# Optimization experiments

Hardware: AMD Instinct MI355X
Metric: run time of the kernel (lower is better)

The kernel has to match this reference:

```python
import jax, jax.numpy as jnp
import numpy as np

B, D_MODEL, N, H = 4, 256, 2048, 4
HEAD_DIM = D_MODEL // H  # 64


def _rotate_half(x):
    # x: [..., d] with d even; pairs (x1, x2) -> (-x2, x1)
    x = x.reshape(x.shape[:-1] + (x.shape[-1] // 2, 2))
    x1, x2 = x[..., 0], x[..., 1]
    return jnp.stack((-x2, x1), axis=-1).reshape(x.shape[:-2] + (-1,))


def _apply_rope(freqs, t):
    # freqs: [2, n, d] (cos, sin); t: [b, h, n, d]
    return t * freqs[0] + _rotate_half(t) * freqs[1]


def setup_inputs() -> dict:
    key = jax.random.key(0)
    ks = jax.random.split(key, 12)
    s = 0.02
    inp = {
        "query": jax.random.normal(ks[0], (B, D_MODEL, N), jnp.float32),
        "key": jax.random.normal(ks[1], (B, D_MODEL, N), jnp.float32),
        "value": jax.random.normal(ks[2], (B, D_MODEL, N), jnp.float32),
        "encoding": jax.random.normal(ks[3], (2, N, HEAD_DIM), jnp.float32),
        "Wq": jax.random.normal(ks[4], (D_MODEL, D_MODEL), jnp.float32) * s,
        "bq": jnp.zeros((D_MODEL,), jnp.float32),
        "Wk": jax.random.normal(ks[5], (D_MODEL, D_MODEL), jnp.float32) * s,
        "bk": jnp.zeros((D_MODEL,), jnp.float32),
        "Wv": jax.random.normal(ks[6], (D_MODEL, D_MODEL), jnp.float32) * s,
        "bv": jnp.zeros((D_MODEL,), jnp.float32),
        "Wm": jax.random.normal(ks[7], (D_MODEL, D_MODEL), jnp.float32) * s,
        "bm": jnp.zeros((D_MODEL,), jnp.float32),
    }
    return inp


def _proj(W, b, x):
    # 1x1 Conv1d == channel matmul: x [b, c_in, n] -> [b, c_out, n]
    return jnp.einsum('oi,bin->bon', W, x) + b[None, :, None]


def reference(query, key, value, encoding, Wq, bq, Wk, bk, Wv, bv, Wm, bm):
    b = query.shape[0]
    # project and split channels into (head_dim, heads): [b, d, h, n]
    q = _proj(Wq, bq, query).reshape(b, HEAD_DIM, H, -1)
    k = _proj(Wk, bk, key).reshape(b, HEAD_DIM, H, -1)
    v = _proj(Wv, bv, value).reshape(b, HEAD_DIM, H, -1)
    # RoPE on [b, h, n, d] layout
    q = jnp.transpose(_apply_rope(encoding, jnp.transpose(q, (0, 2, 3, 1))), (0, 3, 1, 2))
    k = jnp.transpose(_apply_rope(encoding, jnp.transpose(k, (0, 2, 3, 1))), (0, 3, 1, 2))
    # attention: scores [b, h, n, m]
    scores = jnp.einsum('bdhn,bdhm->bhnm', q, k) / jnp.sqrt(jnp.float32(HEAD_DIM))
    prob = jax.nn.softmax(scores, axis=-1)
    x = jnp.einsum('bhnm,bdhm->bdhn', prob, v)
    x = x.reshape(b, HEAD_DIM * H, -1)
    return _proj(Wm, bm, x)
```

## Files before the change

kernel.cpp:

```cpp
#include <hip/hip_runtime.h>
#include <stdint.h>

#define NSEQ 2048

typedef __attribute__((ext_vector_type(4))) float f32x4;
typedef __attribute__((ext_vector_type(8))) short s16x8;
typedef _Float16 f16x8 __attribute__((ext_vector_type(8)));

#define OFF_XT  0u
#define OFF_XA  0u
#define OFF_PO  4194304u
#define OFF_W   12582912u
#define OFF_QR  13107200u
#define OFF_KR  17301504u
#define OFF_VT  21495808u
#define OFF_M   25690112u
#define OFF_L   25952256u

__device__ __forceinline__ short f2h(float f) {
  _Float16 h = (_Float16)f;
  return __builtin_bit_cast(short, h);
}
__device__ __forceinline__ float h2f(short s) {
  return (float)__builtin_bit_cast(_Float16, s);
}
__device__ __forceinline__ int swz64(int row, int slot) {
  return row * 64 + ((slot ^ ((row >> 1) & 3)) << 4);
}
__device__ __forceinline__ int swz128(int row, int slot) {
  return row * 128 + ((slot ^ (row & 7)) << 4);
}
#define MFMA(a, b, c) __builtin_amdgcn_mfma_f32_16x16x32_f16(a, b, c, 0, 0, 0)

__global__ void k_convw(const float* __restrict__ Wq, const float* __restrict__ Wk,
                        const float* __restrict__ Wv, const float* __restrict__ Wm,
                        char* __restrict__ ws) {
  int o = blockIdx.x, which = blockIdx.y, i = threadIdx.x;
  const float* src = which == 0 ? Wq : which == 1 ? Wk : which == 2 ? Wv : Wm;
  short* dst = (short*)(ws + OFF_W) + which * 65536;
  float val = (which < 3) ? src[o * 256 + i] : src[o * 256 + ((i & 63) << 2) + (i >> 6)];
  dst[o * 256 + i] = f2h(val);
}

__global__ __launch_bounds__(256) void k_trans(const float* __restrict__ q,
    const float* __restrict__ k, const float* __restrict__ v, char* __restrict__ ws) {
  int tensor = blockIdx.z >> 2, b = blockIdx.z & 3;
  const float* src = tensor == 0 ? q : (tensor == 1 ? k : v);
  short* dst = (short*)(ws + OFF_XT) + (tensor * 4 + b) * 524288;
  int n0 = blockIdx.x * 64, i0 = blockIdx.y * 64;
  __shared__ float tile[64][65];
  int t = threadIdx.x;
  int nl = t & 63, ib = (t >> 6) * 16;
#pragma unroll
  for (int r = 0; r < 16; ++r)
    tile[ib + r][nl] = src[(b * 256 + i0 + ib + r) * 2048 + n0 + nl];
  __syncthreads();
  int nr = t >> 2, ic = (t & 3) * 16;
  short tmp[16];
#pragma unroll
  for (int j = 0; j < 16; ++j) tmp[j] = f2h(tile[ic + j][nr]);
  short* dp = &dst[(n0 + nr) * 256 + i0 + ic];
  *(s16x8*)dp = *(const s16x8*)&tmp[0];
  *(s16x8*)(dp + 8) = *(const s16x8*)&tmp[8];
}

__device__ __forceinline__ void gemm128(const short* __restrict__ W, const short* __restrict__ X,
                                        int o0, int n0, short* As, short* Bs, f32x4 acc[4][4]) {
  int t = threadIdx.x;
  int lane = t & 63, g = lane >> 4, c = lane & 15, wave = t >> 6;
  int wo = (wave >> 1) * 64, wn = (wave & 1) * 64;
  int row = t >> 2, slot = t & 3;
  for (int kk = 0; kk < 8; ++kk) {
    __syncthreads();
    int koff = kk * 32 + slot * 8;
    *(s16x8*)((char*)As + swz64(row, slot))      = *(const s16x8*)&W[(o0 + row) * 256 + koff];
    *(s16x8*)((char*)As + swz64(row + 64, slot)) = *(const s16x8*)&W[(o0 + row + 64) * 256 + koff];
    *(s16x8*)((char*)Bs + swz64(row, slot))      = *(const s16x8*)&X[(n0 + row) * 256 + koff];
    *(s16x8*)((char*)Bs + swz64(row + 64, slot)) = *(const s16x8*)&X[(n0 + row + 64) * 256 + koff];
    __syncthreads();
    f16x8 af[4], bfr[4];
#pragma unroll
    for (int f = 0; f < 4; ++f) {
      af[f]  = *(const f16x8*)((char*)As + swz64(wo + f * 16 + c, g));
      bfr[f] = *(const f16x8*)((char*)Bs + swz64(wn + f * 16 + c, g));
    }
#pragma unroll
    for (int i = 0; i < 4; ++i)
#pragma unroll
      for (int j = 0; j < 4; ++j)
        acc[i][j] = MFMA(af[i], bfr[j], acc[i][j]);
  }
}

__global__ __launch_bounds__(256) void k_proj(const float* __restrict__ enc,
    const float* __restrict__ bq, const float* __restrict__ bk, const float* __restrict__ bv,
    char* __restrict__ ws) {
  int proj = blockIdx.z >> 2, b = blockIdx.z & 3;
  const short* W = (const short*)(ws + OFF_W) + proj * 65536;
  const short* X = (const short*)(ws + OFF_XT) + (proj * 4 + b) * 524288;
  int o0 = blockIdx.y * 128, n0 = blockIdx.x * 128;
  __shared__ short As[128 * 32], Bs[128 * 32];
  f32x4 acc[4][4] = {};
  gemm128(W, X, o0, n0, As, Bs, acc);
  int t = threadIdx.x, lane = t & 63, g = lane >> 4, c = lane & 15, wave = t >> 6;
  int wo = (wave >> 1) * 64, wn = (wave & 1) * 64;
  const float* bias = proj == 0 ? bq : (proj == 1 ? bk : bv);
  if (proj < 2) {
    short* dst = (short*)(ws + (proj == 0 ? OFF_QR : OFF_KR));
    float scale = proj == 0 ? 0.125f : 1.0f;
    float sgn = (g & 1) ? 1.0f : -1.0f;
#pragma unroll
    for (int i = 0; i < 4; ++i) {
      int ob = o0 + wo + i * 16 + g * 4;
      int d = ob >> 2;
#pragma unroll
      for (int j = 0; j < 4; ++j) {
        int n = n0 + wn + j * 16 + c;
        float cv = enc[n * 64 + d], sv = enc[131072 + n * 64 + d];
#pragma unroll
        for (int r = 0; r < 4; ++r) {
          float val = acc[i][j][r] + bias[ob + r];
          float par = __shfl_xor(val, 16, 64);
          float res = (val * cv + sgn * par * sv) * scale;
          dst[((b * 4 + r) * 2048 + n) * 64 + d] = f2h(res);
        }
      }
    }
  } else {
    short* dst = (short*)(ws + OFF_VT);
#pragma unroll
    for (int i = 0; i < 4; ++i) {
      int ob = o0 + wo + i * 16 + g * 4;
      int d = ob >> 2;
#pragma unroll
      for (int j = 0; j < 4; ++j) {
        int n = n0 + wn + j * 16 + c;
#pragma unroll
        for (int r = 0; r < 4; ++r) {
          float val = acc[i][j][r] + bias[ob + r];
          dst[((b * 4 + r) * 64 + d) * 2048 + n] = f2h(val);
        }
      }
    }
  }
}

__global__ __launch_bounds__(256, 4) void k_attn(char* __restrict__ ws) {
  int bh = blockIdx.y, ms = blockIdx.z;
  int t = threadIdx.x, wave = t >> 6, lane = t & 63, g = lane >> 4, c = lane & 15;
  int nw = blockIdx.x * 64 + wave * 16;
  const short* Q = (const short*)(ws + OFF_QR) + bh * 131072;
  const short* K = (const short*)(ws + OFF_KR) + bh * 131072;
  const short* V = (const short*)(ws + OFF_VT) + bh * 131072;
  __shared__ short Ks[64 * 64], Vs[64 * 64], Ps[4][16 * 64];
  char* Pb = (char*)Ps[wave];
  f16x8 qf0 = *(const f16x8*)&Q[(nw + c) * 64 + g * 8];
  f16x8 qf1 = *(const f16x8*)&Q[(nw + c) * 64 + 32 + g * 8];
  f32x4 po[4] = {};
  float mrun[4], lrun[4];
#pragma unroll
  for (int r = 0; r < 4; ++r) { mrun[r] = -1e30f; lrun[r] = 0.f; }
  int sr = t >> 3, sl = t & 7;
  const int mb = ms * 1024;

  s16x8 rk0, rk1, rv0, rv1, sk0, sk1, sv0, sv1;
  auto LD = [&](int m0, s16x8& a, s16x8& b2, s16x8& c2, s16x8& d2) {
    a  = *(const s16x8*)&K[(m0 + sr) * 64 + sl * 8];
    b2 = *(const s16x8*)&K[(m0 + sr + 32) * 64 + sl * 8];
    c2 = *(const s16x8*)&V[sr * 2048 + m0 + sl * 8];
    d2 = *(const s16x8*)&V[(sr + 32) * 2048 + m0 + sl * 8];
  };
  auto ST = [&](const s16x8& a, const s16x8& b2, const s16x8& c2, const s16x8& d2) {
    *(s16x8*)((char*)Ks + swz128(sr, sl))      = a;
    *(s16x8*)((char*)Ks + swz128(sr + 32, sl)) = b2;
    *(s16x8*)((char*)Vs + swz128(sr, sl))      = c2;
    *(s16x8*)((char*)Vs + swz128(sr + 32, sl)) = d2;
  };
  auto COMPUTE = [&]() {
    f32x4 s[4] = {};
    __builtin_amdgcn_s_setprio(1);
#pragma unroll
    for (int fj = 0; fj < 4; ++fj) {
      f16x8 k0 = *(const f16x8*)((char*)Ks + swz128(fj * 16 + c, g));
      f16x8 k1 = *(const f16x8*)((char*)Ks + swz128(fj * 16 + c, 4 + g));
      s[fj] = MFMA(qf0, k0, s[fj]);
      s[fj] = MFMA(qf1, k1, s[fj]);
    }
    __builtin_amdgcn_s_setprio(0);
    float pm[4], nm[4], corr[4], rs[4];
#pragma unroll
    for (int r = 0; r < 4; ++r) {
      pm[r] = fmaxf(fmaxf(s[0][r], s[1][r]), fmaxf(s[2][r], s[3][r]));
#pragma unroll
      for (int d_ = 1; d_ < 16; d_ <<= 1) pm[r] = fmaxf(pm[r], __shfl_xor(pm[r], d_, 64));
      nm[r] = fmaxf(mrun[r], pm[r]);
      corr[r] = __expf(mrun[r] - nm[r]);
      mrun[r] = nm[r];
      rs[r] = 0.f;
    }
    float p[4][4];
#pragma unroll
    for (int fj = 0; fj < 4; ++fj)
#pragma unroll
      for (int r = 0; r < 4; ++r) {
        p[fj][r] = __expf(s[fj][r] - nm[r]);
        rs[r] += p[fj][r];
      }
#pragma unroll
    for (int r = 0; r < 4; ++r) {
#pragma unroll
      for (int d_ = 1; d_ < 16; d_ <<= 1) rs[r] += __shfl_xor(rs[r], d_, 64);
      lrun[r] = lrun[r] * corr[r] + rs[r];
    }
#pragma unroll
    for (int fd = 0; fd < 4; ++fd)
#pragma unroll
      for (int r = 0; r < 4; ++r) po[fd][r] *= corr[r];
#pragma unroll
    for (int fj = 0; fj < 4; ++fj)
#pragma unroll
      for (int r = 0; r < 4; ++r) {
        int rr = g * 4 + r, mm = fj * 16 + c;
        *(short*)(Pb + swz128(rr, mm >> 3) + (mm & 7) * 2) = f2h(p[fj][r]);
      }
    asm volatile("s_waitcnt lgkmcnt(0)" ::: "memory");
    __builtin_amdgcn_sched_barrier(0);
    f16x8 pa0 = *(const f16x8*)(Pb + swz128(c, g));
    f16x8 pa1 = *(const f16x8*)(Pb + swz128(c, 4 + g));
    __builtin_amdgcn_s_setprio(1);
#pragma unroll
    for (int fd = 0; fd < 4; ++fd) {
      int dd = fd * 16 + c;
      f16x8 vb0 = *(const f16x8*)((char*)Vs + swz128(dd, g));
      f16x8 vb1 = *(const f16x8*)((char*)Vs + swz128(dd, 4 + g));
      po[fd] = MFMA(pa0, vb0, po[fd]);
      po[fd] = MFMA(pa1, vb1, po[fd]);
    }
    __builtin_amdgcn_s_setprio(0);
  };

  LD(mb, rk0, rk1, rv0, rv1);
  for (int tt = 0; tt < 16; tt += 2) {
    __syncthreads();
    ST(rk0, rk1, rv0, rv1);
    LD(mb + (tt + 1) * 64, sk0, sk1, sv0, sv1);
    __syncthreads();
    COMPUTE();
    __syncthreads();
    ST(sk0, sk1, sv0, sv1);
    if (tt + 2 < 16) LD(mb + (tt + 2) * 64, rk0, rk1, rv0, rv1);
    __syncthreads();
    COMPUTE();
  }

  short* PO = (short*)(ws + OFF_PO);
  float* Mm = (float*)(ws + OFF_M);
  float* Ll = (float*)(ws + OFF_L);
  int base = (ms * 16 + bh) * 2048;
#pragma unroll
  for (int fd = 0; fd < 4; ++fd) {
    int d = fd * 16 + c;
#pragma unroll
    for (int r = 0; r < 4; ++r) {
      int n = nw + g * 4 + r;
      PO[(base + n) * 64 + d] = f2h(po[fd][r] / lrun[r]);
    }
  }
  if (c == 0) {
#pragma unroll
    for (int r = 0; r < 4; ++r) {
      int n = nw + g * 4 + r;
      Mm[base + n] = mrun[r];
      Ll[base + n] = lrun[r];
    }
  }
}

__global__ __launch_bounds__(256) void k_comb(char* __restrict__ ws) {
  int t = threadIdx.x;
  int row = blockIdx.x * 32 + (t >> 3);
  int bh = row >> 11, n = row & 2047;
  int dc = (t & 7) * 8;
  const short* PO = (const short*)(ws + OFF_PO);
  const float* Mm = (const float*)(ws + OFF_M);
  const float* Ll = (const float*)(ws + OFF_L);
  float m1 = Mm[row], m2 = Mm[32768 + row];
  float l1 = Ll[row], l2 = Ll[32768 + row];
  float M = fmaxf(m1, m2);
  float w1 = l1 * __expf(m1 - M), w2 = l2 * __expf(m2 - M);
  float inv = 1.f / (w1 + w2);
  float a1 = w1 * inv, a2 = w2 * inv;
  s16x8 o1 = *(const s16x8*)&PO[row * 64 + dc];
  s16x8 o2 = *(const s16x8*)&PO[(32768 + row) * 64 + dc];
  short res[8];
#pragma unroll
  for (int j = 0; j < 8; ++j) res[j] = f2h(a1 * h2f(o1[j]) + a2 * h2f(o2[j]));
  short* XA = (short*)(ws + OFF_XA);
  int b = bh >> 2, h = bh & 3;
  *(s16x8*)&XA[(b * 2048 + n) * 256 + h * 64 + dc] = *(const s16x8*)res;
}

__global__ __launch_bounds__(256) void k_final(const float* __restrict__ bm,
    float* __restrict__ out, char* __restrict__ ws) {
  int b = blockIdx.z;
  const short* W = (const short*)(ws + OFF_W) + 3 * 65536;
  const short* X = (const short*)(ws + OFF_XA) + b * 524288;
  int o0 = blockIdx.y * 128, n0 = blockIdx.x * 128;
  __shared__ short As[128 * 32], Bs[128 * 32];
  f32x4 acc[4][4] = {};
  gemm128(W, X, o0, n0, As, Bs, acc);
  int t = threadIdx.x, lane = t & 63, g = lane >> 4, c = lane & 15, wave = t >> 6;
  int wo = (wave >> 1) * 64, wn = (wave & 1) * 64;
#pragma unroll
  for (int i = 0; i < 4; ++i) {
    int ob = o0 + wo + i * 16 + g * 4;
#pragma unroll
    for (int j = 0; j < 4; ++j) {
      int n = n0 + wn + j * 16 + c;
#pragma unroll
      for (int r = 0; r < 4; ++r)
        out[(b * 256 + ob + r) * 2048 + n] = acc[i][j][r] + bm[ob + r];
    }
  }
}

extern "C" void kernel_launch(void* const* d_in, const int* in_sizes, int n_in,
                              void* d_out, int out_size, void* d_ws, size_t ws_size,
                              hipStream_t stream) {
  (void)in_sizes; (void)n_in; (void)out_size; (void)ws_size;
  const float* q   = (const float*)d_in[0];
  const float* k   = (const float*)d_in[1];
  const float* v   = (const float*)d_in[2];
  const float* enc = (const float*)d_in[3];
  const float* Wq  = (const float*)d_in[4];
  const float* bq  = (const float*)d_in[5];
  const float* Wk  = (const float*)d_in[6];
  const float* bk  = (const float*)d_in[7];
  const float* Wv  = (const float*)d_in[8];
  const float* bv  = (const float*)d_in[9];
  const float* Wm  = (const float*)d_in[10];
  const float* bm  = (const float*)d_in[11];
  char* ws = (char*)d_ws;
  float* out = (float*)d_out;
  hipLaunchKernelGGL(k_convw, dim3(256, 4), dim3(256), 0, stream, Wq, Wk, Wv, Wm, ws);
  hipLaunchKernelGGL(k_trans, dim3(32, 4, 12), dim3(256), 0, stream, q, k, v, ws);
  hipLaunchKernelGGL(k_proj, dim3(16, 2, 12), dim3(256), 0, stream, enc, bq, bk, bv, ws);
  hipLaunchKernelGGL(k_attn, dim3(32, 16, 2), dim3(256), 0, stream, ws);
  hipLaunchKernelGGL(k_comb, dim3(1024), dim3(256), 0, stream, ws);
  hipLaunchKernelGGL(k_final, dim3(16, 2, 4), dim3(256), 0, stream, bm, out, ws);
}
```

Measured before the change: 182.5 us.

## Double-buffer attention K/V tiles, lazy softmax rescale, exp2 domain, coalesced RoPE stores

The attention kernel now keeps two LDS buffers for K/V, so the next tile is stored while the current one is computed, and each pair of tiles needs two barriers instead of four. Softmax works in base 2 by folding log2(e) into the Q scale and using exp2f. It rescales the running max and accumulator only when some row's max grows by more than a threshold, which skips most correction multiplies. The Q/K projection epilogue stages RoPE results through LDS so global writes become 16-byte coalesced vectors. The trade-offs are more LDS per block, possible occupancy loss, and extra barriers in the projection kernel.

```diff
diff --git a/kernel.cpp b/kernel.cpp
--- a/kernel.cpp
+++ b/kernel.cpp
@@ -100,31 +100,41 @@
   const short* X = (const short*)(ws + OFF_XT) + (proj * 4 + b) * 524288;
   int o0 = blockIdx.y * 128, n0 = blockIdx.x * 128;
   __shared__ short As[128 * 32], Bs[128 * 32];
+  __shared__ short Es[128 * 40];
   f32x4 acc[4][4] = {};
   gemm128(W, X, o0, n0, As, Bs, acc);
   int t = threadIdx.x, lane = t & 63, g = lane >> 4, c = lane & 15, wave = t >> 6;
   int wo = (wave >> 1) * 64, wn = (wave & 1) * 64;
   const float* bias = proj == 0 ? bq : (proj == 1 ? bk : bv);
   if (proj < 2) {
-    short* dst = (short*)(ws + (proj == 0 ? OFF_QR : OFF_KR));
-    float scale = proj == 0 ? 0.125f : 1.0f;
+    short* dst0 = (short*)(ws + (proj == 0 ? OFF_QR : OFF_KR));
+    float scale = proj == 0 ? 0.18033688f : 1.0f;
     float sgn = (g & 1) ? 1.0f : -1.0f;
-#pragma unroll
-    for (int i = 0; i < 4; ++i) {
-      int ob = o0 + wo + i * 16 + g * 4;
-      int d = ob >> 2;
-#pragma unroll
-      for (int j = 0; j < 4; ++j) {
-        int n = n0 + wn + j * 16 + c;
-        float cv = enc[n * 64 + d], sv = enc[131072 + n * 64 + d];
-#pragma unroll
-        for (int r = 0; r < 4; ++r) {
+    int d0 = o0 >> 2;
+    int srow = t >> 1, sseg = t & 1;
+#pragma unroll
+    for (int r = 0; r < 4; ++r) {
+      __syncthreads();
+#pragma unroll
+      for (int i = 0; i < 4; ++i) {
+        int ob = o0 + wo + i * 16 + g * 4;
+        int d = ob >> 2;
+        int dl = (wo >> 2) + i * 4 + g;
+#pragma unroll
+        for (int j = 0; j < 4; ++j) {
+          int n = n0 + wn + j * 16 + c;
+          float cv = enc[n * 64 + d], sv = enc[131072 + n * 64 + d];
           float val = acc[i][j][r] + bias[ob + r];
           float par = __shfl_xor(val, 16, 64);
           float res = (val * cv + sgn * par * sv) * scale;
-          dst[((b * 4 + r) * 2048 + n) * 64 + d] = f2h(res);
+          Es[(wn + j * 16 + c) * 40 + dl] = f2h(res);
         }
       }
+      __syncthreads();
+      short* dp = &dst0[((b * 4 + r) * 2048 + n0 + srow) * 64 + d0 + sseg * 16];
+      const short* ep = &Es[srow * 40 + sseg * 16];
+      *(s16x8*)dp = *(const s16x8*)ep;
+      *(s16x8*)(dp + 8) = *(const s16x8*)(ep + 8);
     }
   } else {
     short* dst = (short*)(ws + OFF_VT);
@@ -152,7 +162,7 @@
   const short* Q = (const short*)(ws + OFF_QR) + bh * 131072;
   const short* K = (const short*)(ws + OFF_KR) + bh * 131072;
   const short* V = (const short*)(ws + OFF_VT) + bh * 131072;
-  __shared__ short Ks[64 * 64], Vs[64 * 64], Ps[4][16 * 64];
+  __shared__ short Ks[2][64 * 64], Vs[2][64 * 64], Ps[4][16 * 64];
   char* Pb = (char*)Ps[wave];
   f16x8 qf0 = *(const f16x8*)&Q[(nw + c) * 64 + g * 8];
   f16x8 qf1 = *(const f16x8*)&Q[(nw + c) * 64 + 32 + g * 8];
@@ -163,59 +173,71 @@
   int sr = t >> 3, sl = t & 7;
   const int mb = ms * 1024;
 
-  s16x8 rk0, rk1, rv0, rv1, sk0, sk1, sv0, sv1;
-  auto LD = [&](int m0, s16x8& a, s16x8& b2, s16x8& c2, s16x8& d2) {
-    a  = *(const s16x8*)&K[(m0 + sr) * 64 + sl * 8];
-    b2 = *(const s16x8*)&K[(m0 + sr + 32) * 64 + sl * 8];
-    c2 = *(const s16x8*)&V[sr * 2048 + m0 + sl * 8];
-    d2 = *(const s16x8*)&V[(sr + 32) * 2048 + m0 + sl * 8];
+  s16x8 RA[4], RB[4];
+  auto LD = [&](int m0, s16x8* R) {
+    R[0] = *(const s16x8*)&K[(m0 + sr) * 64 + sl * 8];
+    R[1] = *(const s16x8*)&K[(m0 + sr + 32) * 64 + sl * 8];
+    R[2] = *(const s16x8*)&V[sr * 2048 + m0 + sl * 8];
+    R[3] = *(const s16x8*)&V[(sr + 32) * 2048 + m0 + sl * 8];
   };
-  auto ST = [&](const s16x8& a, const s16x8& b2, const s16x8& c2, const s16x8& d2) {
-    *(s16x8*)((char*)Ks + swz128(sr, sl))      = a;
-    *(s16x8*)((char*)Ks + swz128(sr + 32, sl)) = b2;
-    *(s16x8*)((char*)Vs + swz128(sr, sl))      = c2;
-    *(s16x8*)((char*)Vs + swz128(sr + 32, sl)) = d2;
+  auto ST = [&](int buf, const s16x8* R) {
+    *(s16x8*)((char*)Ks[buf] + swz128(sr, sl))      = R[0];
+    *(s16x8*)((char*)Ks[buf] + swz128(sr + 32, sl)) = R[1];
+    *(s16x8*)((char*)Vs[buf] + swz128(sr, sl))      = R[2];
+    *(s16x8*)((char*)Vs[buf] + swz128(sr + 32, sl)) = R[3];
   };
-  auto COMPUTE = [&]() {
+  auto COMPUTE = [&](int buf) {
+    const char* Kb = (const char*)Ks[buf];
+    const char* Vb = (const char*)Vs[buf];
     f32x4 s[4] = {};
     __builtin_amdgcn_s_setprio(1);
 #pragma unroll
     for (int fj = 0; fj < 4; ++fj) {
-      f16x8 k0 = *(const f16x8*)((char*)Ks + swz128(fj * 16 + c, g));
-      f16x8 k1 = *(const f16x8*)((char*)Ks + swz128(fj * 16 + c, 4 + g));
+      f16x8 k0 = *(const f16x8*)(Kb + swz128(fj * 16 + c, g));
+      f16x8 k1 = *(const f16x8*)(Kb + swz128(fj * 16 + c, 4 + g));
       s[fj] = MFMA(qf0, k0, s[fj]);
       s[fj] = MFMA(qf1, k1, s[fj]);
     }
     __builtin_amdgcn_s_setprio(0);
-    float pm[4], nm[4], corr[4], rs[4];
+    float pm[4], nm[4], rs[4];
 #pragma unroll
     for (int r = 0; r < 4; ++r) {
       pm[r] = fmaxf(fmaxf(s[0][r], s[1][r]), fmaxf(s[2][r], s[3][r]));
 #pragma unroll
       for (int d_ = 1; d_ < 16; d_ <<= 1) pm[r] = fmaxf(pm[r], __shfl_xor(pm[r], d_, 64));
-      nm[r] = fmaxf(mrun[r], pm[r]);
-      corr[r] = __expf(mrun[r] - nm[r]);
-      mrun[r] = nm[r];
-      rs[r] = 0.f;
+    }
+    bool grow = (pm[0] > mrun[0] + 11.5f) || (pm[1] > mrun[1] + 11.5f) ||
+                (pm[2] > mrun[2] + 11.5f) || (pm[3] > mrun[3] + 11.5f);
+    if (__any(grow)) {
+#pragma unroll
+      for (int r = 0; r < 4; ++r) {
+        nm[r] = fmaxf(mrun[r], pm[r]);
+        float corr = exp2f(mrun[r] - nm[r]);
+        mrun[r] = nm[r];
+        lrun[r] *= corr;
+#pragma unroll
+        for (int fd = 0; fd < 4; ++fd) po[fd][r] *= corr;
+      }
+    } else {
+#pragma unroll
+      for (int r = 0; r < 4; ++r) nm[r] = mrun[r];
     }
     float p[4][4];
 #pragma unroll
+    for (int r = 0; r < 4; ++r) rs[r] = 0.f;
+#pragma unroll
     for (int fj = 0; fj < 4; ++fj)
 #pragma unroll
       for (int r = 0; r < 4; ++r) {
-        p[fj][r] = __expf(s[fj][r] - nm[r]);
+        p[fj][r] = exp2f(s[fj][r] - nm[r]);
         rs[r] += p[fj][r];
       }
 #pragma unroll
     for (int r = 0; r < 4; ++r) {
 #pragma unroll
       for (int d_ = 1; d_ < 16; d_ <<= 1) rs[r] += __shfl_xor(rs[r], d_, 64);
-      lrun[r] = lrun[r] * corr[r] + rs[r];
-    }
-#pragma unroll
-    for (int fd = 0; fd < 4; ++fd)
-#pragma unroll
-      for (int r = 0; r < 4; ++r) po[fd][r] *= corr[r];
+      lrun[r] += rs[r];
+    }
 #pragma unroll
     for (int fj = 0; fj < 4; ++fj)
 #pragma unroll
@@ -231,26 +253,29 @@
 #pragma unroll
     for (int fd = 0; fd < 4; ++fd) {
       int dd = fd * 16 + c;
-      f16x8 vb0 = *(const f16x8*)((char*)Vs + swz128(dd, g));
-      f16x8 vb1 = *(const f16x8*)((char*)Vs + swz128(dd, 4 + g));
+      f16x8 vb0 = *(const f16x8*)(Vb + swz128(dd, g));
+      f16x8 vb1 = *(const f16x8*)(Vb + swz128(dd, 4 + g));
       po[fd] = MFMA(pa0, vb0, po[fd]);
       po[fd] = MFMA(pa1, vb1, po[fd]);
     }
     __builtin_amdgcn_s_setprio(0);
   };
 
-  LD(mb, rk0, rk1, rv0, rv1);
+  LD(mb, RA); LD(mb + 64, RB);
+  ST(0, RA);
+  LD(mb + 128, RA);
+  __syncthreads();
   for (int tt = 0; tt < 16; tt += 2) {
+    ST(1, RB);
+    if (tt + 3 < 16) LD(mb + (tt + 3) * 64, RB);
+    COMPUTE(0);
     __syncthreads();
-    ST(rk0, rk1, rv0, rv1);
-    LD(mb + (tt + 1) * 64, sk0, sk1, sv0, sv1);
+    if (tt + 2 < 16) {
+      ST(0, RA);
+      if (tt + 4 < 16) LD(mb + (tt + 4) * 64, RA);
+    }
+    COMPUTE(1);
     __syncthreads();
-    COMPUTE();
-    __syncthreads();
-    ST(sk0, sk1, sv0, sv1);
-    if (tt + 2 < 16) LD(mb + (tt + 2) * 64, rk0, rk1, rv0, rv1);
-    __syncthreads();
-    COMPUTE();
   }
 
   short* PO = (short*)(ws + OFF_PO);
@@ -287,7 +312,7 @@
   float m1 = Mm[row], m2 = Mm[32768 + row];
   float l1 = Ll[row], l2 = Ll[32768 + row];
   float M = fmaxf(m1, m2);
-  float w1 = l1 * __expf(m1 - M), w2 = l2 * __expf(m2 - M);
+  float w1 = l1 * exp2f(m1 - M), w2 = l2 * exp2f(m2 - M);
   float inv = 1.f / (w1 + w2);
   float a1 = w1 * inv, a2 = w2 * inv;
   s16x8 o1 = *(const s16x8*)&PO[row * 64 + dc];
```

Measured after the change: 190.8 us. +4.6%, slower.
